# Kernel optimization log

Measured on AMD Instinct MI355X. Metric: run time of the kernel, lower is better.

## Reference

```python
import jax, jax.numpy as jnp
import numpy as np

N_HEAD = 16


def setup_inputs() -> dict:
    key = jax.random.key(0)
    ks = jax.random.split(key, 5)
    B, T, C = 2, 2048, 1024
    s = 1.0 / np.sqrt(C)
    inp = {
        "x": jax.random.normal(ks[0], (B, T, C), dtype=jnp.float32),
        "Wq": jax.random.normal(ks[1], (C, C), dtype=jnp.float32) * s,
        "bq": jnp.zeros((C,), dtype=jnp.float32),
        "Wk": jax.random.normal(ks[2], (C, C), dtype=jnp.float32) * s,
        "bk": jnp.zeros((C,), dtype=jnp.float32),
        "Wv": jax.random.normal(ks[3], (C, C), dtype=jnp.float32) * s,
        "bv": jnp.zeros((C,), dtype=jnp.float32),
        "Wp": jax.random.normal(ks[4], (C, C), dtype=jnp.float32) * s,
        "bp": jnp.zeros((C,), dtype=jnp.float32),
    }
    return inp


def reference(x, Wq, bq, Wk, bk, Wv, bv, Wp, bp):
    B, T, C = x.shape
    H = N_HEAD
    D = C // H
    # linear projections (torch Linear: x @ W.T + b)
    q = (x @ Wq.T + bq).reshape(B, T, H, D)
    k = (x @ Wk.T + bk).reshape(B, T, H, D)
    v = (x @ Wv.T + bv).reshape(B, T, H, D)
    # scaled dot-product attention (NO causal mask in original forward)
    att = jnp.einsum("bthd,bshd->bhts", q, k) * (1.0 / np.sqrt(D))
    att = jax.nn.softmax(att, axis=-1)
    y = jnp.einsum("bhts,bshd->bthd", att, v).reshape(B, T, C)
    # output projection (dropouts are identity at p=0 / eval)
    return y @ Wp.T + bp
```

## Files before the change

kernel.cpp:

```cpp
#include <hip/hip_runtime.h>
#include <hip/hip_bf16.h>

typedef __attribute__((ext_vector_type(4))) float f32x4;
typedef __attribute__((ext_vector_type(16))) float f32x16;
typedef __attribute__((ext_vector_type(8))) short bf16x8;
typedef __attribute__((ext_vector_type(2))) unsigned int u32x2;

#define T_SEQ 2048
#define C_DIM 1024
#define NH 16
#define DHD 64

__device__ __forceinline__ unsigned cvtpk_bf16(float lo, float hi) {
    unsigned r;
    asm("v_cvt_pk_bf16_f32 %0, %1, %2" : "=v"(r) : "v"(lo), "v"(hi));
    return r;
}

__device__ __forceinline__ float exp2_hw(float x) {
    float r;
    asm("v_exp_f32 %0, %1" : "=v"(r) : "v"(x));
    return r;
}

__device__ __forceinline__ void async_copy16(void* lds, const void* g) {
    __builtin_amdgcn_global_load_lds(
        (const __attribute__((address_space(1))) unsigned int*)(uintptr_t)g,
        (__attribute__((address_space(3))) unsigned int*)(unsigned int)(uintptr_t)lds,
        16, 0, 0);
}

__global__ __launch_bounds__(256) void cvt_all(const float* __restrict__ x,
                                               const float* __restrict__ Wq, const float* __restrict__ Wk,
                                               const float* __restrict__ Wv, const float* __restrict__ Wp,
                                               __hip_bfloat16* __restrict__ xb,
                                               __hip_bfloat16* __restrict__ wf,
                                               __hip_bfloat16* __restrict__ wpb) {
    int i = blockIdx.x * blockDim.x + threadIdx.x;
    const float* src; __hip_bfloat16* dst; int off;
    if (i < 1048576) { src = x; dst = xb; off = i; }
    else {
        int j = i - 1048576; int wi = j >> 18; off = j & 262143;
        switch (wi) {
            case 0:  src = Wq; dst = wf;           break;
            case 1:  src = Wk; dst = wf + 1048576; break;
            case 2:  src = Wv; dst = wf + 2097152; break;
            default: src = Wp; dst = wpb;          break;
        }
    }
    float4 v = *(const float4*)(src + (size_t)off * 4);
    union { __hip_bfloat16 h[4]; u32x2 u; } p;
    p.h[0] = __float2bfloat16(v.x); p.h[1] = __float2bfloat16(v.y);
    p.h[2] = __float2bfloat16(v.z); p.h[3] = __float2bfloat16(v.w);
    *(u32x2*)(dst + (size_t)off * 4) = p.u;
}

__global__ __launch_bounds__(512) void gemm_qkv(const __hip_bfloat16* __restrict__ A,
                                                const __hip_bfloat16* __restrict__ Bw,
                                                const float* __restrict__ biasq,
                                                const float* __restrict__ biask,
                                                const float* __restrict__ biasv,
                                                __hip_bfloat16* __restrict__ oq,
                                                __hip_bfloat16* __restrict__ okk,
                                                __hip_bfloat16* __restrict__ ovt) {
    __shared__ __align__(16) char lds[131072];

    const int wg = ((int)blockIdx.x & 7) * 32 + ((int)blockIdx.x >> 3);
    const int m0 = (wg & 31) * 128;
    const int n0 = (wg >> 5) * 384;

    const int tid = threadIdx.x;
    const int w = tid >> 6, l = tid & 63;
    const int wr = w >> 2, wc = w & 3;
    const int lg = l >> 4, lr = l & 15;

    const int sr0 = tid >> 3;
    const int sc0 = (tid & 7) * 16;
    const int gc0 = sc0 ^ ((sr0 & 7) << 4);
    const size_t goff = (size_t)sr0 * 2048 + gc0;

    const char* Ag = (const char*)A + (size_t)m0 * 2048;
    const char* Bg = (const char*)Bw + (size_t)n0 * 2048;

    auto STAGE_A = [&](int buf, int half, int kt) {
        const char* g = Ag + (size_t)(half * 64) * 2048 + kt * 128 + goff;
        char* d = lds + (buf * 2 + half) * 8192 + w * 1024;
        async_copy16(d, g);
    };
    auto STAGE_B = [&](int buf, int half, int kt) {
        #pragma unroll
        for (int p = 0; p < 3; p++) {
            const char* g = Bg + (size_t)(half * 192 + p * 64) * 2048 + kt * 128 + goff;
            char* d = lds + 32768 + (buf * 2 + half) * 24576 + p * 8192 + w * 1024;
            async_copy16(d, g);
        }
    };

    const int sw = (lr & 7) << 4;
    auto LDA = [&](bf16x8* af, int buf) {
        const char* base = lds + (buf * 2 + wr) * 8192;
        #pragma unroll
        for (int m = 0; m < 4; m++) {
            const int r = m * 16 + lr;
            #pragma unroll
            for (int kk = 0; kk < 2; kk++)
                af[m * 2 + kk] = *(const bf16x8*)(base + r * 128 + ((kk * 64 + lg * 16) ^ sw));
        }
    };
    auto LDB = [&](bf16x8* bfv, int buf, int nq) {
        const char* base = lds + 32768 + (buf * 2 + (wc >> 1)) * 24576;
        #pragma unroll
        for (int n = 0; n < 2; n++) {
            const int r = (wc & 1) * 96 + (nq * 2 + n) * 16 + lr;
            #pragma unroll
            for (int kk = 0; kk < 2; kk++)
                bfv[n * 2 + kk] = *(const bf16x8*)(base + r * 128 + ((kk * 64 + lg * 16) ^ sw));
        }
    };

    f32x4 acc[4][6] = {};
    auto MF = [&](const bf16x8* af, const bf16x8* bfv, int nq) {
        #pragma unroll
        for (int m = 0; m < 4; m++)
            #pragma unroll
            for (int n = 0; n < 2; n++)
                #pragma unroll
                for (int kk = 0; kk < 2; kk++)
                    acc[m][nq * 2 + n] = __builtin_amdgcn_mfma_f32_16x16x32_bf16(
                        af[m * 2 + kk], bfv[n * 2 + kk], acc[m][nq * 2 + n], 0, 0, 0);
    };

#define PH_OPEN()  __builtin_amdgcn_sched_barrier(0); \
                   __builtin_amdgcn_s_barrier(); \
                   asm volatile("s_waitcnt lgkmcnt(0)" ::: "memory"); \
                   __builtin_amdgcn_sched_barrier(0); \
                   __builtin_amdgcn_s_setprio(1);
#define PH_CLOSE() __builtin_amdgcn_s_setprio(0); \
                   __builtin_amdgcn_sched_barrier(0); \
                   __builtin_amdgcn_s_barrier();
#define PH_CLOSE_VM2() __builtin_amdgcn_s_setprio(0); \
                   asm volatile("s_waitcnt vmcnt(2)" ::: "memory"); \
                   __builtin_amdgcn_sched_barrier(0); \
                   __builtin_amdgcn_s_barrier();
#define PH_CLOSE_VM5() __builtin_amdgcn_s_setprio(0); \
                   asm volatile("s_waitcnt vmcnt(5)" ::: "memory"); \
                   __builtin_amdgcn_sched_barrier(0); \
                   __builtin_amdgcn_s_barrier();

    bf16x8 af[8], bfA[4], bfB[4], bfC[4];

    STAGE_B(0, 0, 0); STAGE_B(0, 1, 0); STAGE_A(0, 0, 0); STAGE_A(0, 1, 0);
    STAGE_A(1, 0, 1); STAGE_A(1, 1, 1); STAGE_B(1, 0, 1);
    asm volatile("s_waitcnt vmcnt(5)" ::: "memory");
    __builtin_amdgcn_sched_barrier(0);
    __builtin_amdgcn_s_barrier();

    for (int it = 0; it < 8; ++it) {
        const int t1 = 2 * it + 1;
        const int c2 = (2 * it + 2 < 16) ? 2 * it + 2 : 14;
        const int c3 = (2 * it + 3 < 16) ? 2 * it + 3 : 15;
        const int b2 = c2 & 1, b3 = c3 & 1;

        LDA(af, 0); LDB(bfA, 0, 0);
        STAGE_B(1, 1, t1);
        PH_OPEN(); MF(af, bfA, 0); PH_CLOSE();
        LDB(bfB, 0, 1);
        STAGE_A(b2, 0, c2); STAGE_A(b2, 1, c2);
        PH_OPEN(); MF(af, bfB, 1); PH_CLOSE();
        LDB(bfC, 0, 2);
        PH_OPEN(); MF(af, bfC, 2); PH_CLOSE_VM2();

        LDA(af, 1); LDB(bfA, 1, 0);
        STAGE_B(b2, 0, c2);
        PH_OPEN(); MF(af, bfA, 0); PH_CLOSE();
        LDB(bfB, 1, 1);
        STAGE_B(b2, 1, c2); STAGE_A(b3, 0, c3); STAGE_A(b3, 1, c3);
        PH_OPEN(); MF(af, bfB, 1); PH_CLOSE();
        LDB(bfC, 1, 2);
        STAGE_B(b3, 0, c3);
        PH_OPEN(); MF(af, bfC, 2); PH_CLOSE_VM5();
    }
#undef PH_OPEN
#undef PH_CLOSE
#undef PH_CLOSE_VM2
#undef PH_CLOSE_VM5

    #pragma unroll
    for (int m = 0; m < 4; m++) {
        const int rowb = m0 + wr * 64 + m * 16 + lg * 4;
        const int b = rowb >> 11, t0r = rowb & 2047;
        #pragma unroll
        for (int nf = 0; nf < 6; nf++) {
            const int col = n0 + wc * 96 + nf * 16 + lr;
            const int proj = col >> 10;
            const int colL = col & 1023;
            const int hh = colL >> 6, dd = colL & 63;
            if (proj < 2) {
                const float* bias = (proj == 0) ? biasq : biask;
                const float bsc = (proj == 0) ? 0.125f * 1.4426950408889634f : 1.0f;
                __hip_bfloat16* dst = (proj == 0) ? oq : okk;
                #pragma unroll
                for (int rr = 0; rr < 4; rr++) {
                    const int row = rowb + rr;
                    float val = (acc[m][nf][rr] + bias[colL]) * bsc;
                    dst[(((size_t)(b * NH + hh)) * T_SEQ + (row & 2047)) * DHD + dd] = __float2bfloat16(val);
                }
            } else {
                const float bv = biasv[colL];
                union { __hip_bfloat16 h[4]; u32x2 u; } p;
                #pragma unroll
                for (int rr = 0; rr < 4; rr++)
                    p.h[rr] = __float2bfloat16(acc[m][nf][rr] + bv);
                *(u32x2*)&ovt[(((size_t)(b * NH + hh)) * DHD + dd) * T_SEQ + t0r] = p.u;
            }
        }
    }
}

__global__ __launch_bounds__(512) void gemm_proj2(const __hip_bfloat16* __restrict__ A,
                                                  const __hip_bfloat16* __restrict__ Bw,
                                                  const float* __restrict__ biasp,
                                                  float* __restrict__ outf) {
    __shared__ __align__(16) char lds[65536];

    const int wg = ((int)blockIdx.x & 7) * 32 + ((int)blockIdx.x >> 3);
    const int m0 = (wg & 31) * 128;
    const int n0 = (wg >> 5) * 128;

    const int tid = threadIdx.x;
    const int w = tid >> 6, l = tid & 63;
    const int wr = w >> 2, wc = w & 3;
    const int lg = l >> 4, lr = l & 15;

    const int sr0 = tid >> 3;
    const int sc0 = (tid & 7) * 16;
    const int gc0 = sc0 ^ ((sr0 & 7) << 4);
    const size_t goff = (size_t)sr0 * 2048 + gc0;

    const char* Ag = (const char*)A + (size_t)m0 * 2048;
    const char* Bg = (const char*)Bw + (size_t)n0 * 2048;

    auto STAGE_A = [&](int buf, int half, int kt) {
        const char* g = Ag + (size_t)(half * 64) * 2048 + kt * 128 + goff;
        char* d = lds + (buf * 2 + half) * 8192 + w * 1024;
        async_copy16(d, g);
    };
    auto STAGE_B = [&](int buf, int half, int kt) {
        const char* g = Bg + (size_t)(half * 64) * 2048 + kt * 128 + goff;
        char* d = lds + 32768 + (buf * 2 + half) * 8192 + w * 1024;
        async_copy16(d, g);
    };

    const int sw = (lr & 7) << 4;
    auto LDA = [&](bf16x8* af, int buf) {
        const char* base = lds + (buf * 2 + wr) * 8192;
        #pragma unroll
        for (int m = 0; m < 4; m++) {
            const int r = m * 16 + lr;
            #pragma unroll
            for (int kk = 0; kk < 2; kk++)
                af[m * 2 + kk] = *(const bf16x8*)(base + r * 128 + ((kk * 64 + lg * 16) ^ sw));
        }
    };
    auto LDB = [&](bf16x8* bfv, int buf, int n) {
        const char* base = lds + 32768 + (buf * 2 + (wc >> 1)) * 8192;
        const int r = (wc & 1) * 32 + n * 16 + lr;
        #pragma unroll
        for (int kk = 0; kk < 2; kk++)
            bfv[kk] = *(const bf16x8*)(base + r * 128 + ((kk * 64 + lg * 16) ^ sw));
    };

    f32x4 acc[4][2] = {};
    auto MF = [&](const bf16x8* af, const bf16x8* bfv, int n) {
        #pragma unroll
        for (int m = 0; m < 4; m++)
            #pragma unroll
            for (int kk = 0; kk < 2; kk++)
                acc[m][n] = __builtin_amdgcn_mfma_f32_16x16x32_bf16(
                    af[m * 2 + kk], bfv[kk], acc[m][n], 0, 0, 0);
    };

#define PH_OPEN()  __builtin_amdgcn_sched_barrier(0); \
                   __builtin_amdgcn_s_barrier(); \
                   asm volatile("s_waitcnt lgkmcnt(0)" ::: "memory"); \
                   __builtin_amdgcn_sched_barrier(0); \
                   __builtin_amdgcn_s_setprio(1);
#define PH_CLOSE() __builtin_amdgcn_s_setprio(0); \
                   __builtin_amdgcn_sched_barrier(0); \
                   __builtin_amdgcn_s_barrier();
#define PH_CLOSE_VM2() __builtin_amdgcn_s_setprio(0); \
                   asm volatile("s_waitcnt vmcnt(2)" ::: "memory"); \
                   __builtin_amdgcn_sched_barrier(0); \
                   __builtin_amdgcn_s_barrier();

    bf16x8 af[8], bf0[2], bf1[2];

    STAGE_B(0, 0, 0); STAGE_B(0, 1, 0); STAGE_A(0, 0, 0); STAGE_A(0, 1, 0);
    STAGE_A(1, 0, 1); STAGE_A(1, 1, 1);
    asm volatile("s_waitcnt vmcnt(2)" ::: "memory");
    __builtin_amdgcn_sched_barrier(0);
    __builtin_amdgcn_s_barrier();

    for (int it = 0; it < 8; ++it) {
        const int t1 = 2 * it + 1;
        const int c2 = (2 * it + 2 < 16) ? 2 * it + 2 : 14;
        const int c3 = (2 * it + 3 < 16) ? 2 * it + 3 : 15;
        const int b2 = c2 & 1, b3 = c3 & 1;

        LDA(af, 0); LDB(bf0, 0, 0);
        STAGE_B(1, 0, t1); STAGE_B(1, 1, t1);
        PH_OPEN(); MF(af, bf0, 0); PH_CLOSE();
        LDB(bf1, 0, 1);
        STAGE_A(b2, 0, c2); STAGE_A(b2, 1, c2);
        PH_OPEN(); MF(af, bf1, 1); PH_CLOSE_VM2();

        LDA(af, 1); LDB(bf0, 1, 0);
        STAGE_B(b2, 0, c2); STAGE_B(b2, 1, c2);
        PH_OPEN(); MF(af, bf0, 0); PH_CLOSE();
        LDB(bf1, 1, 1);
        STAGE_A(b3, 0, c3); STAGE_A(b3, 1, c3);
        PH_OPEN(); MF(af, bf1, 1); PH_CLOSE_VM2();
    }
#undef PH_OPEN
#undef PH_CLOSE
#undef PH_CLOSE_VM2

    #pragma unroll
    for (int m = 0; m < 4; m++)
        #pragma unroll
        for (int n = 0; n < 2; n++)
            #pragma unroll
            for (int r = 0; r < 4; r++) {
                int row = m0 + wr * 64 + m * 16 + lg * 4 + r;
                int col = n0 + wc * 32 + n * 16 + lr;
                outf[(size_t)row * C_DIM + col] = acc[m][n][r] + biasp[col];
            }
}

__global__ __launch_bounds__(256) void attn8(const __hip_bfloat16* __restrict__ Q,
                                             const __hip_bfloat16* __restrict__ K,
                                             const __hip_bfloat16* __restrict__ Vt,
                                             __hip_bfloat16* __restrict__ Y) {
    const int bid = blockIdx.x;
    const int xcd = bid & 7, slot = bid >> 3;
    const int head = xcd * 4 + (slot & 3);
    const int qblk = slot >> 2;

    const int tid = threadIdx.x;
    const int w = tid >> 6, l = tid & 63;
    const int lq = l & 31, hi = l >> 5;
    const int q0 = qblk * 128 + w * 32;

    __shared__ __align__(16) char Ks[3][8192];
    __shared__ __align__(16) char Vs[3][8192];
    __shared__ float bc[4][32];

    const char* Kb = (const char*)(K + (size_t)head * T_SEQ * DHD);
    const char* Vb = (const char*)(Vt + (size_t)head * DHD * T_SEQ);

    bf16x8 qf[4];
    {
        const char* qrow = (const char*)(Q + ((size_t)head * T_SEQ + q0 + lq) * DHD);
        #pragma unroll
        for (int t = 0; t < 4; t++) qf[t] = *(const bf16x8*)(qrow + t * 32 + hi * 16);
    }

    f32x16 yacc[2] = {};
    float ls0 = 0.f, ls1 = 0.f, ls2 = 0.f, ls3 = 0.f;

    const int o0 = (2 * w) * 1024 + l * 16;
    const int o1 = o0 + 1024;
    const int r0 = o0 >> 7, c0b = o0 & 127;
    const int r1 = o1 >> 7, c1b = o1 & 127;
    const int wads0 = r0 * 128 + (c0b ^ ((r0 & 7) << 4));
    const int wads1 = r1 * 128 + (c1b ^ ((r1 & 7) << 4));
    const char* vsrc0 = Vb + (size_t)r0 * (T_SEQ * 2) + c0b;
    const char* vsrc1 = Vb + (size_t)r1 * (T_SEQ * 2) + c1b;

    float4 kreg0, kreg1, vreg0, vreg1;
    auto stage_load = [&](int tile) {
        const char* kb2 = Kb + (size_t)tile * 8192;
        kreg0 = *(const float4*)(kb2 + o0);
        kreg1 = *(const float4*)(kb2 + o1);
        vreg0 = *(const float4*)(vsrc0 + (size_t)tile * 128);
        vreg1 = *(const float4*)(vsrc1 + (size_t)tile * 128);
    };
    auto stage_write = [&](int buf) {
        *(float4*)(&Ks[buf][wads0]) = kreg0;
        *(float4*)(&Ks[buf][wads1]) = kreg1;
        *(float4*)(&Vs[buf][wads0]) = vreg0;
        *(float4*)(&Vs[buf][wads1]) = vreg1;
    };

    auto qk = [&](int buf, f32x16& s0h, f32x16& s1h) {
        s0h = f32x16{}; s1h = f32x16{};
        const char* base0 = Ks[buf] + lq * 128;
        const char* base1 = Ks[buf] + (32 + lq) * 128;
        const int sw0 = (lq & 7) << 4;
        __builtin_amdgcn_s_setprio(1);
        #pragma unroll
        for (int t = 0; t < 4; t++) {
            bf16x8 kf0 = *(const bf16x8*)(base0 + ((t * 32 + hi * 16) ^ sw0));
            s0h = __builtin_amdgcn_mfma_f32_32x32x16_bf16(kf0, qf[t], s0h, 0, 0, 0);
        }
        #pragma unroll
        for (int t = 0; t < 4; t++) {
            bf16x8 kf1 = *(const bf16x8*)(base1 + ((t * 32 + hi * 16) ^ sw0));
            s1h = __builtin_amdgcn_mfma_f32_32x32x16_bf16(kf1, qf[t], s1h, 0, 0, 0);
        }
        __builtin_amdgcn_s_setprio(0);
    };

    auto sm_exp = [&](f32x16& a, f32x16& b) {
        #pragma unroll
        for (int r = 0; r < 16; r += 4) {
            a[r + 0] = exp2_hw(a[r + 0]); a[r + 1] = exp2_hw(a[r + 1]);
            a[r + 2] = exp2_hw(a[r + 2]); a[r + 3] = exp2_hw(a[r + 3]);
            b[r + 0] = exp2_hw(b[r + 0]); b[r + 1] = exp2_hw(b[r + 1]);
            b[r + 2] = exp2_hw(b[r + 2]); b[r + 3] = exp2_hw(b[r + 3]);
            ls0 += a[r + 0] + b[r + 0];
            ls1 += a[r + 1] + b[r + 1];
            ls2 += a[r + 2] + b[r + 2];
            ls3 += a[r + 3] + b[r + 3];
        }
    };

    auto pv = [&](int buf, const f32x16& a, const f32x16& b) {
        unsigned pw0[8], pw1[8];
        #pragma unroll
        for (int M = 0; M < 4; M++) {
            const int u = M * 4;
            pw0[M] = cvtpk_bf16(a[u + 0], a[u + 1]);
            pw1[M] = cvtpk_bf16(a[u + 2], a[u + 3]);
            pw0[M + 4] = cvtpk_bf16(b[u + 0], b[u + 1]);
            pw1[M + 4] = cvtpk_bf16(b[u + 2], b[u + 3]);
        }
        __builtin_amdgcn_s_setprio(1);
        #pragma unroll
        for (int t = 0; t < 4; t++) {
            u32x2 s0p = __builtin_amdgcn_permlane32_swap(pw0[2 * t], pw0[2 * t + 1], false, false);
            u32x2 s1p = __builtin_amdgcn_permlane32_swap(pw1[2 * t], pw1[2 * t + 1], false, false);
            union { unsigned u[4]; bf16x8 v; } af;
            af.u[0] = s0p.x; af.u[1] = s1p.x; af.u[2] = s0p.y; af.u[3] = s1p.y;
            #pragma unroll
            for (int dh = 0; dh < 2; dh++) {
                const int row = dh * 32 + lq;
                bf16x8 vf = *(const bf16x8*)(&Vs[buf][row * 128 + ((t * 32 + hi * 16) ^ ((row & 7) << 4))]);
                yacc[dh] = __builtin_amdgcn_mfma_f32_32x32x16_bf16(af.v, vf, yacc[dh], 0, 0, 0);
            }
        }
        __builtin_amdgcn_s_setprio(0);
    };

    f32x16 sA0, sA1, sB0, sB1;
    stage_load(0); stage_write(0);
    stage_load(1); stage_write(1);
    stage_load(2);
    __syncthreads();
    qk(0, sA0, sA1);

    for (int t = 0; t < 32; t += 2) {
        qk((t + 1) % 3, sB0, sB1);
        if (t + 2 < 32) {
            asm volatile("s_waitcnt vmcnt(0)" ::: "memory");
            stage_write((t + 2) % 3);
            if (t + 3 < 32) stage_load(t + 3);
        }
        sm_exp(sA0, sA1);
        pv(t % 3, sA0, sA1);
        asm volatile("s_waitcnt lgkmcnt(0)" ::: "memory");
        __builtin_amdgcn_s_barrier();
        __builtin_amdgcn_sched_barrier(0);

        const int t1 = t + 1;
        if (t1 + 1 < 32) qk((t1 + 1) % 3, sA0, sA1);
        if (t1 + 2 < 32) {
            asm volatile("s_waitcnt vmcnt(0)" ::: "memory");
            stage_write((t1 + 2) % 3);
            if (t1 + 3 < 32) stage_load(t1 + 3);
        }
        sm_exp(sB0, sB1);
        pv(t1 % 3, sB0, sB1);
        asm volatile("s_waitcnt lgkmcnt(0)" ::: "memory");
        __builtin_amdgcn_s_barrier();
        __builtin_amdgcn_sched_barrier(0);
    }

    float lsum = (ls0 + ls1) + (ls2 + ls3);
    lsum += __shfl_xor(lsum, 32);
    float inv = 1.0f / lsum;
    if (hi == 0) bc[w][lq] = inv;
    asm volatile("s_waitcnt lgkmcnt(0)" ::: "memory");
    __builtin_amdgcn_sched_barrier(0);

    const int b = head >> 4, h16 = head & 15;
    const size_t rowbase = (size_t)b * T_SEQ + q0;
    #pragma unroll
    for (int r = 0; r < 16; r++) {
        const int crow = (r & 3) + 8 * (r >> 2) + 4 * hi;
        const float iv = bc[w][crow];
        const size_t row = rowbase + crow;
        Y[row * C_DIM + h16 * DHD + lq]      = __float2bfloat16(yacc[0][r] * iv);
        Y[row * C_DIM + h16 * DHD + 32 + lq] = __float2bfloat16(yacc[1][r] * iv);
    }
}

extern "C" void kernel_launch(void* const* d_in, const int* in_sizes, int n_in,
                              void* d_out, int out_size, void* d_ws, size_t ws_size,
                              hipStream_t stream) {
    (void)in_sizes; (void)n_in; (void)out_size; (void)ws_size;
    const float* x  = (const float*)d_in[0];
    const float* Wq = (const float*)d_in[1];
    const float* bq = (const float*)d_in[2];
    const float* Wk = (const float*)d_in[3];
    const float* bk = (const float*)d_in[4];
    const float* Wv = (const float*)d_in[5];
    const float* bv = (const float*)d_in[6];
    const float* Wp = (const float*)d_in[7];
    const float* bp = (const float*)d_in[8];
    float* out = (float*)d_out;

    char* ws = (char*)d_ws;
    const size_t MC = (size_t)4096 * C_DIM;
    const size_t CC = (size_t)C_DIM * C_DIM;
    __hip_bfloat16* xb  = (__hip_bfloat16*)ws;  ws += MC * 2;
    __hip_bfloat16* wf  = (__hip_bfloat16*)ws;  ws += 3 * CC * 2;
    __hip_bfloat16* wpb = (__hip_bfloat16*)ws;  ws += CC * 2;
    __hip_bfloat16* qb  = (__hip_bfloat16*)ws;  ws += MC * 2;
    __hip_bfloat16* kb  = (__hip_bfloat16*)ws;  ws += MC * 2;
    __hip_bfloat16* vtb = (__hip_bfloat16*)ws;  ws += MC * 2;
    __hip_bfloat16* yb  = (__hip_bfloat16*)ws;  ws += MC * 2;

    cvt_all<<<8192, 256, 0, stream>>>(x, Wq, Wk, Wv, Wp, xb, wf, wpb);

    gemm_qkv<<<256, 512, 0, stream>>>(xb, wf, bq, bk, bv, qb, kb, vtb);

    attn8<<<512, 256, 0, stream>>>(qb, kb, vtb, yb);

    gemm_proj2<<<256, 512, 0, stream>>>(yb, wpb, bp, out);
}
```

Baseline: 113.0 us.

## Restructure attention KV pipeline to process tile pairs with double-buffered pairs

The attention kernel's K/V staging changes from a three-buffer ring with one tile per half-iteration to a four-buffer scheme that loads and writes two tiles at a time. Each loop iteration now computes both QK products up front, then runs the softmax-exp and PV for both tiles, with one barrier per pair instead of one per tile. The goal is fewer barriers and more latency hiding per sync. The cost is more shared memory (64 KB versus 48 KB) and twice as many staging registers, which may reduce occupancy. The previous overlap of one tile's QK with the prior tile's PV is also lost.

After: 120.6 us. 6.7% more time.

```diff
diff --git a/kernel.cpp b/kernel.cpp
--- a/kernel.cpp
+++ b/kernel.cpp
@@ -337,10 +337,10 @@
             }
 }
 
-__global__ __launch_bounds__(256) void attn8(const __hip_bfloat16* __restrict__ Q,
-                                             const __hip_bfloat16* __restrict__ K,
-                                             const __hip_bfloat16* __restrict__ Vt,
-                                             __hip_bfloat16* __restrict__ Y) {
+__global__ __launch_bounds__(256) void attn11(const __hip_bfloat16* __restrict__ Q,
+                                              const __hip_bfloat16* __restrict__ K,
+                                              const __hip_bfloat16* __restrict__ Vt,
+                                              __hip_bfloat16* __restrict__ Y) {
     const int bid = blockIdx.x;
     const int xcd = bid & 7, slot = bid >> 3;
     const int head = xcd * 4 + (slot & 3);
@@ -351,8 +351,8 @@
     const int lq = l & 31, hi = l >> 5;
     const int q0 = qblk * 128 + w * 32;
 
-    __shared__ __align__(16) char Ks[3][8192];
-    __shared__ __align__(16) char Vs[3][8192];
+    __shared__ __align__(16) char Ks[4][8192];
+    __shared__ __align__(16) char Vs[4][8192];
     __shared__ float bc[4][32];
 
     const char* Kb = (const char*)(K + (size_t)head * T_SEQ * DHD);
@@ -377,19 +377,22 @@
     const char* vsrc0 = Vb + (size_t)r0 * (T_SEQ * 2) + c0b;
     const char* vsrc1 = Vb + (size_t)r1 * (T_SEQ * 2) + c1b;
 
-    float4 kreg0, kreg1, vreg0, vreg1;
-    auto stage_load = [&](int tile) {
-        const char* kb2 = Kb + (size_t)tile * 8192;
-        kreg0 = *(const float4*)(kb2 + o0);
-        kreg1 = *(const float4*)(kb2 + o1);
-        vreg0 = *(const float4*)(vsrc0 + (size_t)tile * 128);
-        vreg1 = *(const float4*)(vsrc1 + (size_t)tile * 128);
-    };
-    auto stage_write = [&](int buf) {
-        *(float4*)(&Ks[buf][wads0]) = kreg0;
-        *(float4*)(&Ks[buf][wads1]) = kreg1;
-        *(float4*)(&Vs[buf][wads0]) = vreg0;
-        *(float4*)(&Vs[buf][wads1]) = vreg1;
+    float4 kA0, kA1, vA0, vA1, kB0, kB1, vB0, vB1;
+    auto load_pair = [&](int tile) {
+        const char* ka = Kb + (size_t)tile * 8192;
+        const char* kb = ka + 8192;
+        kA0 = *(const float4*)(ka + o0);  kA1 = *(const float4*)(ka + o1);
+        kB0 = *(const float4*)(kb + o0);  kB1 = *(const float4*)(kb + o1);
+        vA0 = *(const float4*)(vsrc0 + (size_t)tile * 128);
+        vA1 = *(const float4*)(vsrc1 + (size_t)tile * 128);
+        vB0 = *(const float4*)(vsrc0 + (size_t)(tile + 1) * 128);
+        vB1 = *(const float4*)(vsrc1 + (size_t)(tile + 1) * 128);
+    };
+    auto write_pair = [&](int base) {
+        *(float4*)(&Ks[base][wads0]) = kA0;  *(float4*)(&Ks[base][wads1]) = kA1;
+        *(float4*)(&Vs[base][wads0]) = vA0;  *(float4*)(&Vs[base][wads1]) = vA1;
+        *(float4*)(&Ks[base + 1][wads0]) = kB0;  *(float4*)(&Ks[base + 1][wads1]) = kB1;
+        *(float4*)(&Vs[base + 1][wads0]) = vB0;  *(float4*)(&Vs[base + 1][wads1]) = vB1;
     };
 
     auto qk = [&](int buf, f32x16& s0h, f32x16& s1h) {
@@ -453,34 +456,23 @@
     };
 
     f32x16 sA0, sA1, sB0, sB1;
-    stage_load(0); stage_write(0);
-    stage_load(1); stage_write(1);
-    stage_load(2);
+    load_pair(0); write_pair(0);
+    load_pair(2);
     __syncthreads();
-    qk(0, sA0, sA1);
-
-    for (int t = 0; t < 32; t += 2) {
-        qk((t + 1) % 3, sB0, sB1);
-        if (t + 2 < 32) {
+
+    for (int p = 0; p < 16; ++p) {
+        const int base = (p & 1) * 2;
+        qk(base, sA0, sA1);
+        qk(base + 1, sB0, sB1);
+        if (p < 15) {
             asm volatile("s_waitcnt vmcnt(0)" ::: "memory");
-            stage_write((t + 2) % 3);
-            if (t + 3 < 32) stage_load(t + 3);
+            write_pair(base ^ 2);
+            if (p < 14) load_pair(2 * p + 4);
         }
         sm_exp(sA0, sA1);
-        pv(t % 3, sA0, sA1);
-        asm volatile("s_waitcnt lgkmcnt(0)" ::: "memory");
-        __builtin_amdgcn_s_barrier();
-        __builtin_amdgcn_sched_barrier(0);
-
-        const int t1 = t + 1;
-        if (t1 + 1 < 32) qk((t1 + 1) % 3, sA0, sA1);
-        if (t1 + 2 < 32) {
-            asm volatile("s_waitcnt vmcnt(0)" ::: "memory");
-            stage_write((t1 + 2) % 3);
-            if (t1 + 3 < 32) stage_load(t1 + 3);
-        }
+        pv(base, sA0, sA1);
         sm_exp(sB0, sB1);
-        pv(t1 % 3, sB0, sB1);
+        pv(base + 1, sB0, sB1);
         asm volatile("s_waitcnt lgkmcnt(0)" ::: "memory");
         __builtin_amdgcn_s_barrier();
         __builtin_amdgcn_sched_barrier(0);
@@ -535,7 +527,7 @@
 
     gemm_qkv<<<256, 512, 0, stream>>>(xb, wf, bq, bk, bv, qb, kb, vtb);
 
-    attn8<<<512, 256, 0, stream>>>(qb, kb, vtb, yb);
+    attn11<<<512, 256, 0, stream>>>(qb, kb, vtb, yb);
 
     gemm_proj2<<<256, 512, 0, stream>>>(yb, wpb, bp, out);
 }
```
